# Kernel optimization log

Hardware: AMD Instinct MI355X
Metric: run time of the kernel (lower is better)

The kernel has to match this reference:

```python
import jax, jax.numpy as jnp
import numpy as np

B, W, F, H = 2048, 64, 128, 128


def setup_inputs() -> dict:
    key = jax.random.key(0)
    ks = jax.random.split(key, 23)
    n = lambda k, shape: jax.random.normal(k, shape, dtype=jnp.float32) * 0.05
    return dict(
        X=jax.random.normal(ks[0], (B, W, F), dtype=jnp.float32),
        # InputAttention: linear1 (W+2H -> W), linear2 (W -> 1)
        ia_W1=n(ks[1], (W, W + 2 * H)), ia_b1=n(ks[2], (W,)),
        ia_W2=n(ks[3], (1, W)), ia_b2=n(ks[4], (1,)),
        # encoder LSTMCell(F, H)
        enc_Wih=n(ks[5], (4 * H, F)), enc_Whh=n(ks[6], (4 * H, H)),
        enc_bih=n(ks[7], (4 * H,)), enc_bhh=n(ks[8], (4 * H,)),
        # TemporalAttention: linear1 (3H -> H), linear2 (H -> 1)
        ta_W1=n(ks[9], (H, 3 * H)), ta_b1=n(ks[10], (H,)),
        ta_W2=n(ks[11], (1, H)), ta_b2=n(ks[12], (1,)),
        # decoder LSTMCell(1, H)
        dec_Wih=n(ks[13], (4 * H, 1)), dec_Whh=n(ks[14], (4 * H, H)),
        dec_bih=n(ks[15], (4 * H,)), dec_bhh=n(ks[16], (4 * H,)),
        # output heads
        l1_W=n(ks[17], (1, 1 + H)), l1_b=n(ks[18], (1,)),
        l2_W=n(ks[19], (H, 2 * H)), l2_b=n(ks[20], (H,)),
        l3_W=n(ks[21], (1, H)), l3_b=n(ks[22], (1,)),
    )


def _lstm_cell(x, h, c, Wih, Whh, bih, bhh):
    g = x @ Wih.T + bih + h @ Whh.T + bhh
    i, f, gg, o = jnp.split(g, 4, axis=-1)
    c_new = jax.nn.sigmoid(f) * c + jax.nn.sigmoid(i) * jnp.tanh(gg)
    h_new = jax.nn.sigmoid(o) * jnp.tanh(c_new)
    return h_new, c_new


def reference(X, ia_W1, ia_b1, ia_W2, ia_b2,
              enc_Wih, enc_Whh, enc_bih, enc_bhh,
              ta_W1, ta_b1, ta_W2, ta_b2,
              dec_Wih, dec_Whh, dec_bih, dec_bhh,
              l1_W, l1_b, l2_W, l2_b, l3_W, l3_b):
    Bsz, Wlen, Fdim = X.shape
    Hdim = enc_Whh.shape[1]
    Xf = jnp.transpose(X, (2, 0, 1))  # [F, B, W] (feature-major view for input attention)

    # ---- encoder with input attention ----
    def enc_step(carry, xt):  # xt: [B, F]
        h, c = carry
        hr = jnp.broadcast_to(h[None], (Fdim, Bsz, Hdim))
        cr = jnp.broadcast_to(c[None], (Fdim, Bsz, Hdim))
        u = jnp.tanh(jnp.concatenate([Xf, hr, cr], axis=-1) @ ia_W1.T + ia_b1)  # [F,B,W]
        e = u @ ia_W2.T + ia_b2                                                  # [F,B,1]
        alpha = jax.nn.softmax(e, axis=0)[..., 0].T                              # [B,F]
        h_new, c_new = _lstm_cell(alpha * xt, h, c, enc_Wih, enc_Whh, enc_bih, enc_bhh)
        return (h_new, c_new), h_new

    z = jnp.zeros((Bsz, Hdim), dtype=X.dtype)
    (_, _), Hs = jax.lax.scan(enc_step, (z, z), jnp.transpose(X, (1, 0, 2)))  # Hs: [W,B,H]
    # dropout: eval mode (identity)

    # ---- decoder with temporal attention ----
    def dec_step(carry, _):
        d, ds, out = carry
        dr = jnp.broadcast_to(d[None], Hs.shape)
        dsr = jnp.broadcast_to(ds[None], Hs.shape)
        v = jnp.tanh(jnp.concatenate([Hs, dr, dsr], axis=-1) @ ta_W1.T + ta_b1)  # [W,B,H]
        l = v @ ta_W2.T + ta_b2                                                   # [W,B,1]
        beta = jax.nn.softmax(l, axis=0)
        ct = jnp.sum(beta * Hs, axis=0)                                           # [B,H]
        yt = jnp.concatenate([out, ct], axis=-1) @ l1_W.T + l1_b                  # [B,1]
        d_new, ds_new = _lstm_cell(yt, d, ds, dec_Wih, dec_Whh, dec_bih, dec_bhh)
        o = jnp.concatenate([ct, d_new], axis=-1) @ l2_W.T + l2_b
        out_new = jax.nn.sigmoid(o @ l3_W.T + l3_b)                               # [B,1]
        return (d_new, ds_new, out_new), None

    out0 = jnp.zeros((Bsz, 1), dtype=X.dtype)
    (_, _, output), _ = jax.lax.scan(dec_step, (z, z, out0), None, length=Wlen)
    return output
```

## Files before the change

### kernel.cpp

```cpp
#include <hip/hip_runtime.h>
#include <hip/hip_fp16.h>
#include <stdint.h>

typedef unsigned int uint;
typedef unsigned short ushort;

#define NB 2048
#define NW 64
#define NF 128
#define NH 128

typedef __attribute__((ext_vector_type(8))) short s8v;
typedef __attribute__((ext_vector_type(8))) _Float16 h8v;
typedef __attribute__((ext_vector_type(4))) float f4v;

#define MFMA16(a, b, c) __builtin_amdgcn_mfma_f32_16x16x32_bf16((a), (b), (c), 0, 0, 0)
#define MFMAH(a, b, c)  __builtin_amdgcn_mfma_f32_16x16x32_f16((a), (b), (c), 0, 0, 0)

union H8 { h8v v; __half2 h2[4]; uint4 u4; ushort us[8]; };

__device__ __forceinline__ float bfl(uint u){ return __uint_as_float(u << 16); }
__device__ __forceinline__ float bfh(uint u){ return __uint_as_float(u & 0xffff0000u); }
__device__ __forceinline__ ushort f2bf(float f){
  uint u = __float_as_uint(f);
  u += 0x7fffu + ((u >> 16) & 1u);
  return (ushort)(u >> 16);
}
__device__ __forceinline__ float bf2f(ushort s){ return __uint_as_float(((uint)s) << 16); }

__device__ __forceinline__ float fast_tanh(float x){
  float e = __expf(x + x);
  return 1.f - 2.f * __builtin_amdgcn_rcpf(e + 1.f);
}
__device__ __forceinline__ float fast_sig(float x){
  return __builtin_amdgcn_rcpf(1.f + __expf(-x));
}
__device__ __forceinline__ ushort expo_h(float x){
  return __half_as_ushort(__float2half(__expf(x + x)));
}

__device__ __forceinline__ s8v packW(const float* p){
  s8v r;
  #pragma unroll
  for (int i = 0; i < 8; ++i) r[i] = (short)f2bf(p[i]);
  return r;
}

__global__ __launch_bounds__(256) void k_upre(const float* __restrict__ X,
                                              const float* __restrict__ iaW1,
                                              ushort* __restrict__ Eenc){
  __shared__ __align__(16) float sXT[128*68];
  const int tid = threadIdx.x, lane = tid & 63, wave = tid >> 6, g = lane >> 4;
  int b = blockIdx.x;
  const float* Xb = X + (size_t)b*NW*NF;
  for (int i = tid; i < NW*NF; i += 256){
    int j = i >> 7, f = i & 127;
    sXT[f*68 + j] = Xb[i];
  }
  s8v bw[2];
  {
    int w = wave*16 + (lane & 15);
    #pragma unroll
    for (int kb = 0; kb < 2; ++kb) bw[kb] = packW(iaW1 + w*320 + kb*32 + g*8);
  }
  __syncthreads();
  ushort* outb = Eenc + (size_t)b*NF*NW;
  int w = wave*16 + (lane & 15);
  #pragma unroll
  for (int mt = 0; mt < 8; ++mt){
    int f = mt*16 + (lane & 15);
    f4v acc = {0.f,0.f,0.f,0.f};
    #pragma unroll
    for (int kb = 0; kb < 2; ++kb){
      const float* p = &sXT[f*68 + kb*32 + g*8];
      s8v a;
      #pragma unroll
      for (int i = 0; i < 8; ++i) a[i] = (short)f2bf(p[i]);
      acc = MFMA16(a, bw[kb], acc);
    }
    int fr = mt*16 + g*4;
    #pragma unroll
    for (int j = 0; j < 4; ++j) outb[(fr + j)*64 + w] = expo_h(acc[j]);
  }
}

__global__ __launch_bounds__(256) void k_vpre(const ushort* __restrict__ Hsb,
                                              const float* __restrict__ taW1,
                                              ushort* __restrict__ Edec,
                                              ushort* __restrict__ HsT){
  __shared__ __align__(16) ushort sH[64*136];
  const int tid = threadIdx.x, lane = tid & 63, wave = tid >> 6, g = lane >> 4;
  int b = blockIdx.x;
  const ushort* Hb = Hsb + (size_t)b*NW*NH;
  for (int i = tid; i < 1024; i += 256){
    int w = i >> 4, c = i & 15;
    *(uint4*)&sH[w*136 + c*8] = *(const uint4*)(Hb + i*8);
  }
  s8v bw[2][4];
  #pragma unroll
  for (int nt = 0; nt < 2; ++nt){
    int h = wave*32 + nt*16 + (lane & 15);
    #pragma unroll
    for (int kb = 0; kb < 4; ++kb)
      bw[nt][kb] = packW(taW1 + h*384 + kb*32 + g*8);
  }
  __syncthreads();
  ushort* ho = HsT + (size_t)b*NH*NW;
  for (int k = 0; k < 32; ++k){
    int i2 = tid + 256*k;
    int h = i2 >> 6, w2 = i2 & 63;
    ho[i2] = sH[w2*136 + h];
  }
  ushort* outb = Edec + (size_t)b*NW*NH;
  #pragma unroll
  for (int mt = 0; mt < 4; ++mt){
    s8v af[4];
    #pragma unroll
    for (int kb = 0; kb < 4; ++kb)
      af[kb] = *(const s8v*)&sH[(mt*16 + (lane&15))*136 + kb*32 + g*8];
    #pragma unroll
    for (int nt = 0; nt < 2; ++nt){
      f4v acc = {0.f,0.f,0.f,0.f};
      #pragma unroll
      for (int kb = 0; kb < 4; ++kb) acc = MFMA16(af[kb], bw[nt][kb], acc);
      int h = wave*32 + nt*16 + (lane&15);
      int wr = mt*16 + g*4;
      #pragma unroll
      for (int j = 0; j < 4; ++j) outb[(wr + j)*128 + h] = expo_h(acc[j]);
    }
  }
}

__global__ __launch_bounds__(512, 2) void k_enc(
    const float* __restrict__ X, const float* __restrict__ iaW1,
    const float* __restrict__ iab1, const float* __restrict__ iaW2,
    const float* __restrict__ encWih, const float* __restrict__ encWhh,
    const float* __restrict__ encbih, const float* __restrict__ encbhh,
    const ushort* __restrict__ Eenc, ushort* __restrict__ Hsb){
  __shared__ __align__(16) ushort sUp[65536];
  __shared__ __align__(16) ushort sAB[16*264];
  __shared__ __align__(16) ushort uhc_h[8*64];
  __shared__ __align__(16) float  xrow[8*128];

  const int tid = threadIdx.x, lane = tid & 63, wave = tid >> 6, g = lane >> 4;
  const int bbase = blockIdx.x * 8;
  const int n16 = wave*16 + (lane & 15);

  for (int i = tid; i < 16*264; i += 512) sAB[i] = 0;
  {
    const ushort* up0 = Eenc + (size_t)bbase*NF*NW;
    #pragma unroll
    for (int k = 0; k < 16; ++k){
      int c = tid + k*512;
      int f = (c >> 3) & 127, s = c & 7;
      uint4 v = *(const uint4*)(up0 + (size_t)c*8);
      *(uint4*)((char*)sUp + (c>>3)*128 + ((s ^ (f & 7)) << 4)) = v;
    }
  }
  float bias_r[4];
  #pragma unroll
  for (int gg = 0; gg < 4; ++gg)
    bias_r[gg] = encbih[gg*128 + n16] + encbhh[gg*128 + n16];
  float b1_r = iab1[n16 & 63];
  float c_r[4] = {0.f, 0.f, 0.f, 0.f};
  s8v bwC[4][8];
  #pragma unroll
  for (int gg = 0; gg < 4; ++gg){
    int j = gg*128 + n16;
    #pragma unroll
    for (int kc = 0; kc < 8; ++kc){
      const float* p = (kc < 4) ? (encWih + j*128 + kc*32) : (encWhh + j*128 + (kc-4)*32);
      bwC[gg][kc] = packW(p + g*8);
    }
  }
  s8v bwA[8];
  if (wave < 4){
    #pragma unroll
    for (int kc = 0; kc < 8; ++kc){
      int col = (kc < 4) ? (192 + kc*32) : (64 + (kc-4)*32);
      bwA[kc] = packW(iaW1 + n16*320 + col + g*8);
    }
  }
  H8 w2f[2];
  #pragma unroll
  for (int kb = 0; kb < 2; ++kb)
    #pragma unroll
    for (int i = 0; i < 8; ++i)
      w2f[kb].v[i] = (_Float16)iaW2[kb*32 + g*8 + i];
  __syncthreads();

  for (int t = 0; t < NW; ++t){
    {
      const float* Xr = X + ((size_t)(bbase + wave)*NW + t)*NF;
      xrow[wave*128 + lane] = Xr[lane];
      xrow[wave*128 + 64 + lane] = Xr[64 + lane];
    }
    s8v aT[8];
    #pragma unroll
    for (int kc = 0; kc < 8; ++kc)
      aT[kc] = *(const s8v*)((const char*)sAB + (lane&15)*528 + kc*64 + g*16);
    if (wave < 4){
      f4v acc = {0.f,0.f,0.f,0.f};
      #pragma unroll
      for (int kc = 0; kc < 8; ++kc) acc = MFMA16(aT[kc], bwA[kc], acc);
      if (lane < 32){
        int mb = g*4;
        #pragma unroll
        for (int j = 0; j < 4; ++j) uhc_h[(mb+j)*64 + n16] = expo_h(acc[j] + b1_r);
      }
    }
    __syncthreads();

    {
      int bb = wave;
      const char* Eb = (const char*)sUp + bb*16384;
      H8 sv[2];
      #pragma unroll
      for (int kb = 0; kb < 2; ++kb)
        sv[kb].u4 = *(const uint4*)((const char*)uhc_h + bb*128 + kb*64 + g*16);
      __half2 one2 = __float2half2_rn(1.f);
      f4v Mc[8];
      #pragma unroll
      for (int ft = 0; ft < 8; ++ft){
        int f = ft*16 + (lane & 15);
        const char* rowp = Eb + f*128;
        f4v acc = {0.f,0.f,0.f,0.f};
        #pragma unroll
        for (int kb = 0; kb < 2; ++kb){
          H8 e, a;
          e.v = *(const h8v*)(rowp + (((kb*4 + g) ^ (f & 7)) << 4));
          #pragma unroll
          for (int q = 0; q < 4; ++q) a.h2[q] = h2rcp(__hfma2(e.h2[q], sv[kb].h2[q], one2));
          acc = MFMAH(a.v, w2f[kb].v, acc);
        }
        Mc[ft] = acc;
      }
      float xs[8][4]; float ssum = 0.f;
      #pragma unroll
      for (int ft = 0; ft < 8; ++ft)
        #pragma unroll
        for (int r = 0; r < 4; ++r){ float x = __expf(-2.f*Mc[ft][r]); xs[ft][r] = x; ssum += x; }
      ssum += __shfl_xor(ssum, 16, 64);
      ssum += __shfl_xor(ssum, 32, 64);
      float inv = __builtin_amdgcn_rcpf(ssum);
      if ((lane & 15) == 0){
        #pragma unroll
        for (int ft = 0; ft < 8; ++ft){
          int f0 = ft*16 + g*4;
          float4 Xv = *(const float4*)&xrow[bb*128 + f0];
          uint lo = (uint)f2bf(xs[ft][0]*inv*Xv.x) | ((uint)f2bf(xs[ft][1]*inv*Xv.y) << 16);
          uint hi = (uint)f2bf(xs[ft][2]*inv*Xv.z) | ((uint)f2bf(xs[ft][3]*inv*Xv.w) << 16);
          *(uint2*)((char*)sAB + bb*528 + f0*2) = make_uint2(lo, hi);
        }
      }
    }
    __syncthreads();

    s8v aX[4];
    #pragma unroll
    for (int kc = 0; kc < 4; ++kc)
      aX[kc] = *(const s8v*)((const char*)sAB + (lane&15)*528 + kc*64 + g*16);
    __syncthreads();

    {
      f4v acc[4];
      #pragma unroll
      for (int gg = 0; gg < 4; ++gg) acc[gg] = (f4v){0.f,0.f,0.f,0.f};
      #pragma unroll
      for (int kc = 0; kc < 8; ++kc){
        s8v af = (kc < 4) ? aX[kc] : aT[kc];
        #pragma unroll
        for (int gg = 0; gg < 4; ++gg) acc[gg] = MFMA16(af, bwC[gg][kc], acc[gg]);
      }
      if (lane < 32){
        int mb = g*4;
        #pragma unroll
        for (int j = 0; j < 4; ++j){
          int m = mb + j;
          float gi = acc[0][j] + bias_r[0];
          float gf = acc[1][j] + bias_r[1];
          float gg2 = acc[2][j] + bias_r[2];
          float go = acc[3][j] + bias_r[3];
          float cold = c_r[j];
          float cn = fast_sig(gf)*cold + fast_sig(gi)*fast_tanh(gg2);
          float hn = fast_sig(go)*fast_tanh(cn);
          c_r[j] = cn;
          sAB[m*264 + n16] = f2bf(cn);
          sAB[m*264 + 128 + n16] = f2bf(hn);
          Hsb[((size_t)(bbase + m)*NW + t)*NH + n16] = f2bf(hn);
        }
      }
    }
    __syncthreads();
  }
}

__global__ __launch_bounds__(512, 2) void k_dec(
    const float* __restrict__ taW1, const float* __restrict__ tab1,
    const float* __restrict__ taW2,
    const float* __restrict__ decWih, const float* __restrict__ decWhh,
    const float* __restrict__ decbih, const float* __restrict__ decbhh,
    const float* __restrict__ l1W, const float* __restrict__ l1b,
    const float* __restrict__ l2W, const float* __restrict__ l2b,
    const float* __restrict__ l3W, const float* __restrict__ l3b,
    const ushort* __restrict__ Edec, const ushort* __restrict__ HsT,
    float* __restrict__ out){
  __shared__ __align__(16) ushort sVp[65536];
  __shared__ __align__(16) ushort sAB[16*264];
  __shared__ __align__(16) ushort sCT[16*136];
  __shared__ __align__(16) ushort vd_h[8*128];
  __shared__ __align__(16) ushort lb_bf[8*64];
  __shared__ __align__(16) float  op_s[8][8];
  __shared__ __align__(16) float  yt_s[8];

  const int tid = threadIdx.x, lane = tid & 63, wave = tid >> 6, g = lane >> 4;
  const int bbase = blockIdx.x * 8;
  const int n16 = wave*16 + (lane & 15);

  for (int i = tid; i < 16*264; i += 512) sAB[i] = 0;
  for (int i = tid; i < 16*136; i += 512) sCT[i] = 0;
  {
    const ushort* vp0 = Edec + (size_t)bbase*NW*NH;
    #pragma unroll
    for (int k = 0; k < 16; ++k){
      int c = tid + k*512;
      int w = (c >> 4) & 63, s = c & 15;
      uint4 v = *(const uint4*)(vp0 + (size_t)c*8);
      *(uint4*)((char*)sVp + (c >> 4)*256 + ((s ^ (w & 15)) << 4)) = v;
    }
  }
  float bias_r[4], wih_r[4];
  #pragma unroll
  for (int gg = 0; gg < 4; ++gg){
    bias_r[gg] = decbih[gg*128 + n16] + decbhh[gg*128 + n16];
    wih_r[gg]  = decWih[gg*128 + n16];
  }
  float tab1_r = tab1[n16];
  float l2b_r  = l2b[n16];
  float l3w_r  = l3W[n16];
  float l1w0 = l1W[0], l1b0 = l1b[0], l3b0 = l3b[0];
  float cds_r[4] = {0.f, 0.f, 0.f, 0.f};
  s8v bwA[8];
  #pragma unroll
  for (int kc = 0; kc < 8; ++kc)
    bwA[kc] = packW(taW1 + n16*384 + 128 + kc*32 + g*8);
  s8v bwD[4][4];
  #pragma unroll
  for (int gg = 0; gg < 4; ++gg){
    int j = gg*128 + n16;
    #pragma unroll
    for (int kc = 0; kc < 4; ++kc)
      bwD[gg][kc] = packW(decWhh + j*128 + kc*32 + g*8);
  }
  s8v bwF[8];
  #pragma unroll
  for (int kc = 0; kc < 8; ++kc)
    bwF[kc] = packW(l2W + n16*256 + kc*32 + g*8);
  H8 w2df[4];
  #pragma unroll
  for (int kb = 0; kb < 4; ++kb)
    #pragma unroll
    for (int i = 0; i < 8; ++i)
      w2df[kb].v[i] = (_Float16)taW2[kb*32 + g*8 + i];
  float l1w[8];
  #pragma unroll
  for (int ht = 0; ht < 8; ++ht) l1w[ht] = l1W[1 + ht*16 + (lane & 15)];
  __syncthreads();

  for (int t = 0; t < NW; ++t){
    s8v aT[8];
    #pragma unroll
    for (int kc = 0; kc < 8; ++kc)
      aT[kc] = *(const s8v*)((const char*)sAB + (lane&15)*528 + kc*64 + g*16);
    {
      f4v acc = {0.f,0.f,0.f,0.f};
      #pragma unroll
      for (int kc = 0; kc < 8; ++kc) acc = MFMA16(aT[kc], bwA[kc], acc);
      if (lane < 32){
        int mb = g*4;
        #pragma unroll
        for (int j = 0; j < 4; ++j) vd_h[(mb+j)*128 + n16] = expo_h(acc[j] + tab1_r);
      }
    }
    __syncthreads();

    {
      int bb = wave;
      const ushort* hb = HsT + (size_t)(bbase + bb)*NH*NW;
      s8v hbf[8][2];
      #pragma unroll
      for (int ht = 0; ht < 8; ++ht){
        int h = ht*16 + (lane & 15);
        #pragma unroll
        for (int kb = 0; kb < 2; ++kb)
          hbf[ht][kb] = *(const s8v*)(hb + h*64 + kb*32 + g*8);
      }
      const char* Eb = (const char*)sVp + bb*16384;
      H8 sv[4];
      #pragma unroll
      for (int kb = 0; kb < 4; ++kb)
        sv[kb].u4 = *(const uint4*)((const char*)vd_h + bb*256 + kb*64 + g*16);
      __half2 one2 = __float2half2_rn(1.f);
      f4v Mc[4];
      #pragma unroll
      for (int wt = 0; wt < 4; ++wt){
        int w = wt*16 + (lane & 15);
        const char* rowp = Eb + w*256;
        f4v acc = {0.f,0.f,0.f,0.f};
        #pragma unroll
        for (int kb = 0; kb < 4; ++kb){
          H8 e, a;
          e.v = *(const h8v*)(rowp + (((kb*4 + g) ^ (w & 15)) << 4));
          #pragma unroll
          for (int q = 0; q < 4; ++q) a.h2[q] = h2rcp(__hfma2(e.h2[q], sv[kb].h2[q], one2));
          acc = MFMAH(a.v, w2df[kb].v, acc);
        }
        Mc[wt] = acc;
      }
      float xs[4][4]; float ssum = 0.f;
      #pragma unroll
      for (int wt = 0; wt < 4; ++wt)
        #pragma unroll
        for (int r = 0; r < 4; ++r){ float x = __expf(-2.f*Mc[wt][r]); xs[wt][r] = x; ssum += x; }
      ssum += __shfl_xor(ssum, 16, 64);
      ssum += __shfl_xor(ssum, 32, 64);
      float inv = __builtin_amdgcn_rcpf(ssum);
      if ((lane & 15) == 0){
        #pragma unroll
        for (int wt = 0; wt < 4; ++wt){
          int w0 = wt*16 + g*4;
          uint lo = (uint)f2bf(xs[wt][0]*inv) | ((uint)f2bf(xs[wt][1]*inv) << 16);
          uint hi = (uint)f2bf(xs[wt][2]*inv) | ((uint)f2bf(xs[wt][3]*inv) << 16);
          *(uint2*)((char*)lb_bf + bb*128 + w0*2) = make_uint2(lo, hi);
        }
      }
      s8v ba[2];
      #pragma unroll
      for (int kb = 0; kb < 2; ++kb)
        ba[kb] = *(const s8v*)((const char*)lb_bf + bb*128 + kb*64 + g*16);
      float p = 0.f;
      #pragma unroll
      for (int ht = 0; ht < 8; ++ht){
        f4v acc = {0.f,0.f,0.f,0.f};
        #pragma unroll
        for (int kb = 0; kb < 2; ++kb) acc = MFMA16(ba[kb], hbf[ht][kb], acc);
        float ctv = acc[0];
        if (lane < 16) sCT[bb*136 + ht*16 + (lane&15)] = f2bf(ctv);
        p += l1w[ht] * ctv;
      }
      p += __shfl_xor(p, 1, 64);
      p += __shfl_xor(p, 2, 64);
      p += __shfl_xor(p, 4, 64);
      p += __shfl_xor(p, 8, 64);
      if (lane == 0) yt_s[bb] = p + l1b0;
    }
    __syncthreads();

    {
      f4v g4[4];
      #pragma unroll
      for (int gg = 0; gg < 4; ++gg) g4[gg] = (f4v){0.f,0.f,0.f,0.f};
      #pragma unroll
      for (int kc = 0; kc < 4; ++kc){
        #pragma unroll
        for (int gg = 0; gg < 4; ++gg) g4[gg] = MFMA16(aT[kc], bwD[gg][kc], g4[gg]);
      }
      if (lane < 32){
        int mb = g*4;
        float4 so = make_float4(0.f, 0.f, 0.f, 0.f);
        #pragma unroll
        for (int w = 0; w < 8; ++w){
          float4 v = *(const float4*)((const char*)op_s + w*32 + g*16);
          so.x += v.x; so.y += v.y; so.z += v.z; so.w += v.w;
        }
        float soa[4] = {so.x, so.y, so.z, so.w};
        #pragma unroll
        for (int j = 0; j < 4; ++j){
          int m = mb + j;
          float outp = (t == 0) ? 0.f : fast_sig(soa[j] + l3b0);
          float yt = yt_s[m] + l1w0*outp;
          float gi = g4[0][j] + bias_r[0] + wih_r[0]*yt;
          float gf = g4[1][j] + bias_r[1] + wih_r[1]*yt;
          float gg2 = g4[2][j] + bias_r[2] + wih_r[2]*yt;
          float go = g4[3][j] + bias_r[3] + wih_r[3]*yt;
          float cold = cds_r[j];
          float cn = fast_sig(gf)*cold + fast_sig(gi)*fast_tanh(gg2);
          float hn = fast_sig(go)*fast_tanh(cn);
          cds_r[j] = cn;
          sAB[m*264 + n16] = f2bf(hn);
          sAB[m*264 + 128 + n16] = f2bf(cn);
        }
      }
    }
    __syncthreads();

    {
      f4v of = {0.f,0.f,0.f,0.f};
      #pragma unroll
      for (int kc = 0; kc < 4; ++kc){
        s8v af = *(const s8v*)((const char*)sCT + (lane&15)*272 + kc*64 + g*16);
        of = MFMA16(af, bwF[kc], of);
      }
      #pragma unroll
      for (int kc = 4; kc < 8; ++kc){
        s8v af = *(const s8v*)((const char*)sAB + (lane&15)*528 + (kc-4)*64 + g*16);
        of = MFMA16(af, bwF[kc], of);
      }
      float p0 = l3w_r*(of[0] + l2b_r);
      float p1 = l3w_r*(of[1] + l2b_r);
      float p2 = l3w_r*(of[2] + l2b_r);
      float p3 = l3w_r*(of[3] + l2b_r);
      #pragma unroll
      for (int off = 1; off <= 8; off <<= 1){
        p0 += __shfl_xor(p0, off, 64);
        p1 += __shfl_xor(p1, off, 64);
        p2 += __shfl_xor(p2, off, 64);
        p3 += __shfl_xor(p3, off, 64);
      }
      if ((lane & 15) == 0 && lane < 32){
        *(float4*)((char*)op_s + wave*32 + g*16) = make_float4(p0, p1, p2, p3);
      }
    }
  }
  __syncthreads();
  if (tid < 8){
    float s = 0.f;
    #pragma unroll
    for (int w = 0; w < 8; ++w) s += op_s[w][tid];
    out[bbase + tid] = fast_sig(s + l3b0);
  }
}

extern "C" void kernel_launch(void* const* d_in, const int* in_sizes, int n_in,
                              void* d_out, int out_size, void* d_ws, size_t ws_size,
                              hipStream_t stream){
  const float* X      = (const float*)d_in[0];
  const float* iaW1   = (const float*)d_in[1];
  const float* iab1   = (const float*)d_in[2];
  const float* iaW2   = (const float*)d_in[3];
  const float* encWih = (const float*)d_in[5];
  const float* encWhh = (const float*)d_in[6];
  const float* encbih = (const float*)d_in[7];
  const float* encbhh = (const float*)d_in[8];
  const float* taW1   = (const float*)d_in[9];
  const float* tab1   = (const float*)d_in[10];
  const float* taW2   = (const float*)d_in[11];
  const float* decWih = (const float*)d_in[13];
  const float* decWhh = (const float*)d_in[14];
  const float* decbih = (const float*)d_in[15];
  const float* decbhh = (const float*)d_in[16];
  const float* l1W    = (const float*)d_in[17];
  const float* l1b    = (const float*)d_in[18];
  const float* l2W    = (const float*)d_in[19];
  const float* l2b    = (const float*)d_in[20];
  const float* l3W    = (const float*)d_in[21];
  const float* l3b    = (const float*)d_in[22];

  char* ws = (char*)d_ws;
  ushort* Eenc = (ushort*)(ws);
  ushort* Hsb  = (ushort*)(ws + 33554432);
  ushort* HsT  = (ushort*)(ws + 2*33554432);
  ushort* Edec = Eenc;

  k_upre<<<dim3(2048), dim3(256), 0, stream>>>(X, iaW1, Eenc);
  k_enc<<<dim3(256), dim3(512), 0, stream>>>(X, iaW1, iab1, iaW2,
                                             encWih, encWhh, encbih, encbhh,
                                             Eenc, Hsb);
  k_vpre<<<dim3(2048), dim3(256), 0, stream>>>(Hsb, taW1, Edec, HsT);
  k_dec<<<dim3(256), dim3(512), 0, stream>>>(taW1, tab1, taW2,
                                             decWih, decWhh, decbih, decbhh,
                                             l1W, l1b, l2W, l2b, l3W, l3b,
                                             Edec, HsT, (float*)d_out);
}
```

Before: 1.153 ms.

## Prefetch next X row, drop a barrier, hoist Hs fragments in decoder

```diff
diff --git a/kernel.cpp b/kernel.cpp
--- a/kernel.cpp
+++ b/kernel.cpp
@@ -19,14 +19,11 @@
 
 union H8 { h8v v; __half2 h2[4]; uint4 u4; ushort us[8]; };
 
-__device__ __forceinline__ float bfl(uint u){ return __uint_as_float(u << 16); }
-__device__ __forceinline__ float bfh(uint u){ return __uint_as_float(u & 0xffff0000u); }
 __device__ __forceinline__ ushort f2bf(float f){
   uint u = __float_as_uint(f);
   u += 0x7fffu + ((u >> 16) & 1u);
   return (ushort)(u >> 16);
 }
-__device__ __forceinline__ float bf2f(ushort s){ return __uint_as_float(((uint)s) << 16); }
 
 __device__ __forceinline__ float fast_tanh(float x){
   float e = __expf(x + x);
@@ -139,6 +136,7 @@
     const ushort* __restrict__ Eenc, ushort* __restrict__ Hsb){
   __shared__ __align__(16) ushort sUp[65536];
   __shared__ __align__(16) ushort sAB[16*264];
+  __shared__ __align__(16) ushort sXt[16*264];
   __shared__ __align__(16) ushort uhc_h[8*64];
   __shared__ __align__(16) float  xrow[8*128];
 
@@ -146,7 +144,7 @@
   const int bbase = blockIdx.x * 8;
   const int n16 = wave*16 + (lane & 15);
 
-  for (int i = tid; i < 16*264; i += 512) sAB[i] = 0;
+  for (int i = tid; i < 16*264; i += 512){ sAB[i] = 0; sXt[i] = 0; }
   {
     const ushort* up0 = Eenc + (size_t)bbase*NF*NW;
     #pragma unroll
@@ -187,13 +185,20 @@
     #pragma unroll
     for (int i = 0; i < 8; ++i)
       w2f[kb].v[i] = (_Float16)iaW2[kb*32 + g*8 + i];
+  {
+    const float* Xr = X + ((size_t)(bbase + wave)*NW + 0)*NF;
+    xrow[wave*128 + lane] = Xr[lane];
+    xrow[wave*128 + 64 + lane] = Xr[64 + lane];
+  }
   __syncthreads();
 
   for (int t = 0; t < NW; ++t){
-    {
-      const float* Xr = X + ((size_t)(bbase + wave)*NW + t)*NF;
-      xrow[wave*128 + lane] = Xr[lane];
-      xrow[wave*128 + 64 + lane] = Xr[64 + lane];
+    float xn0, xn1;
+    {
+      int tn = (t + 1) & 63;
+      const float* Xr = X + ((size_t)(bbase + wave)*NW + tn)*NF;
+      xn0 = Xr[lane];
+      xn1 = Xr[64 + lane];
     }
     s8v aT[8];
     #pragma unroll
@@ -250,19 +255,17 @@
           float4 Xv = *(const float4*)&xrow[bb*128 + f0];
           uint lo = (uint)f2bf(xs[ft][0]*inv*Xv.x) | ((uint)f2bf(xs[ft][1]*inv*Xv.y) << 16);
           uint hi = (uint)f2bf(xs[ft][2]*inv*Xv.z) | ((uint)f2bf(xs[ft][3]*inv*Xv.w) << 16);
-          *(uint2*)((char*)sAB + bb*528 + f0*2) = make_uint2(lo, hi);
+          *(uint2*)((char*)sXt + bb*528 + f0*2) = make_uint2(lo, hi);
         }
       }
     }
     __syncthreads();
 
-    s8v aX[4];
-    #pragma unroll
-    for (int kc = 0; kc < 4; ++kc)
-      aX[kc] = *(const s8v*)((const char*)sAB + (lane&15)*528 + kc*64 + g*16);
-    __syncthreads();
-
-    {
+    {
+      s8v aX[4];
+      #pragma unroll
+      for (int kc = 0; kc < 4; ++kc)
+        aX[kc] = *(const s8v*)((const char*)sXt + (lane&15)*528 + kc*64 + g*16);
       f4v acc[4];
       #pragma unroll
       for (int gg = 0; gg < 4; ++gg) acc[gg] = (f4v){0.f,0.f,0.f,0.f};
@@ -290,6 +293,8 @@
           Hsb[((size_t)(bbase + m)*NW + t)*NH + n16] = f2bf(hn);
         }
       }
+      xrow[wave*128 + lane] = xn0;
+      xrow[wave*128 + 64 + lane] = xn1;
     }
     __syncthreads();
   }
@@ -310,6 +315,7 @@
   __shared__ __align__(16) ushort sCT[16*136];
   __shared__ __align__(16) ushort vd_h[8*128];
   __shared__ __align__(16) ushort lb_bf[8*64];
+  __shared__ __align__(16) ushort sW2h[128];
   __shared__ __align__(16) float  op_s[8][8];
   __shared__ __align__(16) float  yt_s[8];
 
@@ -319,6 +325,7 @@
 
   for (int i = tid; i < 16*264; i += 512) sAB[i] = 0;
   for (int i = tid; i < 16*136; i += 512) sCT[i] = 0;
+  if (tid < 128) sW2h[tid] = __half_as_ushort(__float2half(taW2[tid]));
   {
     const ushort* vp0 = Edec + (size_t)bbase*NW*NH;
     #pragma unroll
@@ -356,15 +363,20 @@
   #pragma unroll
   for (int kc = 0; kc < 8; ++kc)
     bwF[kc] = packW(l2W + n16*256 + kc*32 + g*8);
-  H8 w2df[4];
-  #pragma unroll
-  for (int kb = 0; kb < 4; ++kb)
-    #pragma unroll
-    for (int i = 0; i < 8; ++i)
-      w2df[kb].v[i] = (_Float16)taW2[kb*32 + g*8 + i];
   float l1w[8];
   #pragma unroll
   for (int ht = 0; ht < 8; ++ht) l1w[ht] = l1W[1 + ht*16 + (lane & 15)];
+  s8v hbf[8][2];
+  {
+    const ushort* hb = HsT + (size_t)(bbase + wave)*NH*NW;
+    #pragma unroll
+    for (int ht = 0; ht < 8; ++ht){
+      int h = ht*16 + (lane & 15);
+      #pragma unroll
+      for (int kb = 0; kb < 2; ++kb)
+        hbf[ht][kb] = *(const s8v*)(hb + h*64 + kb*32 + g*8);
+    }
+  }
   __syncthreads();
 
   for (int t = 0; t < NW; ++t){
@@ -386,15 +398,6 @@
 
     {
       int bb = wave;
-      const ushort* hb = HsT + (size_t)(bbase + bb)*NH*NW;
-      s8v hbf[8][2];
-      #pragma unroll
-      for (int ht = 0; ht < 8; ++ht){
-        int h = ht*16 + (lane & 15);
-        #pragma unroll
-        for (int kb = 0; kb < 2; ++kb)
-          hbf[ht][kb] = *(const s8v*)(hb + h*64 + kb*32 + g*8);
-      }
       const char* Eb = (const char*)sVp + bb*16384;
       H8 sv[4];
       #pragma unroll
@@ -409,11 +412,12 @@
         f4v acc = {0.f,0.f,0.f,0.f};
         #pragma unroll
         for (int kb = 0; kb < 4; ++kb){
-          H8 e, a;
+          H8 e, a, wv;
+          wv.u4 = *(const uint4*)&sW2h[kb*32 + g*8];
           e.v = *(const h8v*)(rowp + (((kb*4 + g) ^ (w & 15)) << 4));
           #pragma unroll
           for (int q = 0; q < 4; ++q) a.h2[q] = h2rcp(__hfma2(e.h2[q], sv[kb].h2[q], one2));
-          acc = MFMAH(a.v, w2df[kb].v, acc);
+          acc = MFMAH(a.v, wv.v, acc);
         }
         Mc[wt] = acc;
       }
```

After: 1.229 ms. 1.07x slower.

## Store attention exponent tables in FP8 to halve LDS and raise occupancy

Applied to the files above, without the earlier changes.

```diff
diff --git a/kernel.cpp b/kernel.cpp
--- a/kernel.cpp
+++ b/kernel.cpp
@@ -4,6 +4,7 @@
 
 typedef unsigned int uint;
 typedef unsigned short ushort;
+typedef unsigned char uchar;
 
 #define NB 2048
 #define NW 64
@@ -13,11 +14,14 @@
 typedef __attribute__((ext_vector_type(8))) short s8v;
 typedef __attribute__((ext_vector_type(8))) _Float16 h8v;
 typedef __attribute__((ext_vector_type(4))) float f4v;
+typedef __attribute__((ext_vector_type(2))) float f2v;
+typedef __attribute__((ext_vector_type(2))) _Float16 h2v;
+typedef __attribute__((ext_vector_type(2))) __fp16 p2v;
 
 #define MFMA16(a, b, c) __builtin_amdgcn_mfma_f32_16x16x32_bf16((a), (b), (c), 0, 0, 0)
 #define MFMAH(a, b, c)  __builtin_amdgcn_mfma_f32_16x16x32_f16((a), (b), (c), 0, 0, 0)
 
-union H8 { h8v v; __half2 h2[4]; uint4 u4; ushort us[8]; };
+union H8 { h8v v; __half2 h2[4]; h2v hx[4]; p2v px[4]; uint4 u4; ushort us[8]; };
 
 __device__ __forceinline__ float bfl(uint u){ return __uint_as_float(u << 16); }
 __device__ __forceinline__ float bfh(uint u){ return __uint_as_float(u & 0xffff0000u); }
@@ -26,7 +30,6 @@
   u += 0x7fffu + ((u >> 16) & 1u);
   return (ushort)(u >> 16);
 }
-__device__ __forceinline__ float bf2f(ushort s){ return __uint_as_float(((uint)s) << 16); }
 
 __device__ __forceinline__ float fast_tanh(float x){
   float e = __expf(x + x);
@@ -35,8 +38,24 @@
 __device__ __forceinline__ float fast_sig(float x){
   return __builtin_amdgcn_rcpf(1.f + __expf(-x));
 }
-__device__ __forceinline__ ushort expo_h(float x){
-  return __half_as_ushort(__float2half(__expf(x + x)));
+__device__ __forceinline__ ushort expo_hm(float x){
+  return __half_as_ushort(__float2half(__expf(x + x - 1.f)));
+}
+__device__ __forceinline__ uchar expo_fp8(float x){
+  float e = __expf(x + x + 1.f);
+  return (uchar)(__builtin_amdgcn_cvt_pk_fp8_f32(e, e, 0, false) & 0xff);
+}
+__device__ __forceinline__ H8 fp8x8_to_h8(uint2 ev){
+  H8 r;
+  f2v a = __builtin_amdgcn_cvt_pk_f32_fp8((int)ev.x, false);
+  f2v b = __builtin_amdgcn_cvt_pk_f32_fp8((int)ev.x, true);
+  f2v c = __builtin_amdgcn_cvt_pk_f32_fp8((int)ev.y, false);
+  f2v d = __builtin_amdgcn_cvt_pk_f32_fp8((int)ev.y, true);
+  r.px[0] = __builtin_amdgcn_cvt_pkrtz(a.x, a.y);
+  r.px[1] = __builtin_amdgcn_cvt_pkrtz(b.x, b.y);
+  r.px[2] = __builtin_amdgcn_cvt_pkrtz(c.x, c.y);
+  r.px[3] = __builtin_amdgcn_cvt_pkrtz(d.x, d.y);
+  return r;
 }
 
 __device__ __forceinline__ s8v packW(const float* p){
@@ -48,7 +67,7 @@
 
 __global__ __launch_bounds__(256) void k_upre(const float* __restrict__ X,
                                               const float* __restrict__ iaW1,
-                                              ushort* __restrict__ Eenc){
+                                              uchar* __restrict__ Eenc){
   __shared__ __align__(16) float sXT[128*68];
   const int tid = threadIdx.x, lane = tid & 63, wave = tid >> 6, g = lane >> 4;
   int b = blockIdx.x;
@@ -64,7 +83,7 @@
     for (int kb = 0; kb < 2; ++kb) bw[kb] = packW(iaW1 + w*320 + kb*32 + g*8);
   }
   __syncthreads();
-  ushort* outb = Eenc + (size_t)b*NF*NW;
+  uchar* outb = Eenc + (size_t)b*NF*NW;
   int w = wave*16 + (lane & 15);
   #pragma unroll
   for (int mt = 0; mt < 8; ++mt){
@@ -80,13 +99,13 @@
     }
     int fr = mt*16 + g*4;
     #pragma unroll
-    for (int j = 0; j < 4; ++j) outb[(fr + j)*64 + w] = expo_h(acc[j]);
+    for (int j = 0; j < 4; ++j) outb[(fr + j)*64 + w] = expo_fp8(acc[j]);
   }
 }
 
 __global__ __launch_bounds__(256) void k_vpre(const ushort* __restrict__ Hsb,
                                               const float* __restrict__ taW1,
-                                              ushort* __restrict__ Edec,
+                                              uchar* __restrict__ Edec,
                                               ushort* __restrict__ HsT){
   __shared__ __align__(16) ushort sH[64*136];
   const int tid = threadIdx.x, lane = tid & 63, wave = tid >> 6, g = lane >> 4;
@@ -111,7 +130,7 @@
     int h = i2 >> 6, w2 = i2 & 63;
     ho[i2] = sH[w2*136 + h];
   }
-  ushort* outb = Edec + (size_t)b*NW*NH;
+  uchar* outb = Edec + (size_t)b*NW*NH;
   #pragma unroll
   for (int mt = 0; mt < 4; ++mt){
     s8v af[4];
@@ -126,35 +145,35 @@
       int h = wave*32 + nt*16 + (lane&15);
       int wr = mt*16 + g*4;
       #pragma unroll
-      for (int j = 0; j < 4; ++j) outb[(wr + j)*128 + h] = expo_h(acc[j]);
-    }
-  }
-}
-
-__global__ __launch_bounds__(512, 2) void k_enc(
+      for (int j = 0; j < 4; ++j) outb[(wr + j)*128 + h] = expo_fp8(acc[j]);
+    }
+  }
+}
+
+__global__ __launch_bounds__(512, 4) void k_enc(
     const float* __restrict__ X, const float* __restrict__ iaW1,
     const float* __restrict__ iab1, const float* __restrict__ iaW2,
     const float* __restrict__ encWih, const float* __restrict__ encWhh,
     const float* __restrict__ encbih, const float* __restrict__ encbhh,
-    const ushort* __restrict__ Eenc, ushort* __restrict__ Hsb){
-  __shared__ __align__(16) ushort sUp[65536];
-  __shared__ __align__(16) ushort sAB[16*264];
+    const uchar* __restrict__ Eenc, ushort* __restrict__ Hsb){
+  __shared__ __align__(16) uchar  sUp[65536];
+  __shared__ __align__(16) ushort sAB[16*392];
   __shared__ __align__(16) ushort uhc_h[8*64];
-  __shared__ __align__(16) float  xrow[8*128];
+  __shared__ __align__(16) ushort xrowb[8*128];
 
   const int tid = threadIdx.x, lane = tid & 63, wave = tid >> 6, g = lane >> 4;
   const int bbase = blockIdx.x * 8;
   const int n16 = wave*16 + (lane & 15);
 
-  for (int i = tid; i < 16*264; i += 512) sAB[i] = 0;
+  for (int i = tid; i < 16*392; i += 512) sAB[i] = 0;
   {
-    const ushort* up0 = Eenc + (size_t)bbase*NF*NW;
-    #pragma unroll
-    for (int k = 0; k < 16; ++k){
+    const uchar* up0 = Eenc + (size_t)bbase*NF*NW;
+    #pragma unroll
+    for (int k = 0; k < 8; ++k){
       int c = tid + k*512;
-      int f = (c >> 3) & 127, s = c & 7;
-      uint4 v = *(const uint4*)(up0 + (size_t)c*8);
-      *(uint4*)((char*)sUp + (c>>3)*128 + ((s ^ (f & 7)) << 4)) = v;
+      int row = c >> 2, f = row & 127, s = c & 3;
+      uint4 v = *(const uint4*)(up0 + (size_t)c*16);
+      *(uint4*)((char*)sUp + row*64 + ((s ^ (f & 3)) << 4)) = v;
     }
   }
   float bias_r[4];
@@ -187,18 +206,25 @@
     #pragma unroll
     for (int i = 0; i < 8; ++i)
       w2f[kb].v[i] = (_Float16)iaW2[kb*32 + g*8 + i];
+  {
+    const float* Xr = X + ((size_t)(bbase + wave)*NW + 0)*NF;
+    xrowb[wave*128 + lane] = f2bf(Xr[lane]);
+    xrowb[wave*128 + 64 + lane] = f2bf(Xr[64 + lane]);
+  }
   __syncthreads();
 
   for (int t = 0; t < NW; ++t){
+    float xn0, xn1;
     {
-      const float* Xr = X + ((size_t)(bbase + wave)*NW + t)*NF;
-      xrow[wave*128 + lane] = Xr[lane];
-      xrow[wave*128 + 64 + lane] = Xr[64 + lane];
+      int tn = (t + 1) & 63;
+      const float* Xr = X + ((size_t)(bbase + wave)*NW + tn)*NF;
+      xn0 = Xr[lane];
+      xn1 = Xr[64 + lane];
     }
     s8v aT[8];
     #pragma unroll
     for (int kc = 0; kc < 8; ++kc)
-      aT[kc] = *(const s8v*)((const char*)sAB + (lane&15)*528 + kc*64 + g*16);
+      aT[kc] = *(const s8v*)((const char*)sAB + (lane&15)*784 + kc*64 + g*16);
     if (wave < 4){
       f4v acc = {0.f,0.f,0.f,0.f};
       #pragma unroll
@@ -206,14 +232,14 @@
       if (lane < 32){
         int mb = g*4;
         #pragma unroll
-        for (int j = 0; j < 4; ++j) uhc_h[(mb+j)*64 + n16] = expo_h(acc[j] + b1_r);
+        for (int j = 0; j < 4; ++j) uhc_h[(mb+j)*64 + n16] = expo_hm(acc[j] + b1_r);
       }
     }
     __syncthreads();
 
     {
       int bb = wave;
-      const char* Eb = (const char*)sUp + bb*16384;
+      const char* Eb = (const char*)sUp + bb*8192;
       H8 sv[2];
       #pragma unroll
       for (int kb = 0; kb < 2; ++kb)
@@ -223,12 +249,14 @@
       #pragma unroll
       for (int ft = 0; ft < 8; ++ft){
         int f = ft*16 + (lane & 15);
-        const char* rowp = Eb + f*128;
+        const char* rowp = Eb + f*64;
         f4v acc = {0.f,0.f,0.f,0.f};
         #pragma unroll
         for (int kb = 0; kb < 2; ++kb){
-          H8 e, a;
-          e.v = *(const h8v*)(rowp + (((kb*4 + g) ^ (f & 7)) << 4));
+          int gr = kb*4 + g;
+          uint2 ev = *(const uint2*)(rowp + ((((gr >> 1) ^ (f & 3)) << 4) + ((gr & 1) << 3)));
+          H8 e = fp8x8_to_h8(ev);
+          H8 a;
           #pragma unroll
           for (int q = 0; q < 4; ++q) a.h2[q] = h2rcp(__hfma2(e.h2[q], sv[kb].h2[q], one2));
           acc = MFMAH(a.v, w2f[kb].v, acc);
@@ -247,22 +275,20 @@
         #pragma unroll
         for (int ft = 0; ft < 8; ++ft){
           int f0 = ft*16 + g*4;
-          float4 Xv = *(const float4*)&xrow[bb*128 + f0];
-          uint lo = (uint)f2bf(xs[ft][0]*inv*Xv.x) | ((uint)f2bf(xs[ft][1]*inv*Xv.y) << 16);
-          uint hi = (uint)f2bf(xs[ft][2]*inv*Xv.z) | ((uint)f2bf(xs[ft][3]*inv*Xv.w) << 16);
-          *(uint2*)((char*)sAB + bb*528 + f0*2) = make_uint2(lo, hi);
+          uint2 xw = *(const uint2*)&xrowb[bb*128 + f0];
+          uint lo = (uint)f2bf(xs[ft][0]*inv*bfl(xw.x)) | ((uint)f2bf(xs[ft][1]*inv*bfh(xw.x)) << 16);
+          uint hi = (uint)f2bf(xs[ft][2]*inv*bfl(xw.y)) | ((uint)f2bf(xs[ft][3]*inv*bfh(xw.y)) << 16);
+          *(uint2*)((char*)sAB + bb*784 + 512 + f0*2) = make_uint2(lo, hi);
         }
       }
     }
     __syncthreads();
 
-    s8v aX[4];
-    #pragma unroll
-    for (int kc = 0; kc < 4; ++kc)
-      aX[kc] = *(const s8v*)((const char*)sAB + (lane&15)*528 + kc*64 + g*16);
-    __syncthreads();
-
     {
+      s8v aX[4];
+      #pragma unroll
+      for (int kc = 0; kc < 4; ++kc)
+        aX[kc] = *(const s8v*)((const char*)sAB + (lane&15)*784 + 512 + kc*64 + g*16);
       f4v acc[4];
       #pragma unroll
       for (int gg = 0; gg < 4; ++gg) acc[gg] = (f4v){0.f,0.f,0.f,0.f};
@@ -285,17 +311,19 @@
           float cn = fast_sig(gf)*cold + fast_sig(gi)*fast_tanh(gg2);
           float hn = fast_sig(go)*fast_tanh(cn);
           c_r[j] = cn;
-          sAB[m*264 + n16] = f2bf(cn);
-          sAB[m*264 + 128 + n16] = f2bf(hn);
+          sAB[m*392 + n16] = f2bf(cn);
+          sAB[m*392 + 128 + n16] = f2bf(hn);
           Hsb[((size_t)(bbase + m)*NW + t)*NH + n16] = f2bf(hn);
         }
       }
+      xrowb[wave*128 + lane] = f2bf(xn0);
+      xrowb[wave*128 + 64 + lane] = f2bf(xn1);
     }
     __syncthreads();
   }
 }
 
-__global__ __launch_bounds__(512, 2) void k_dec(
+__global__ __launch_bounds__(512, 4) void k_dec(
     const float* __restrict__ taW1, const float* __restrict__ tab1,
     const float* __restrict__ taW2,
     const float* __restrict__ decWih, const float* __restrict__ decWhh,
@@ -303,11 +331,11 @@
     const float* __restrict__ l1W, const float* __restrict__ l1b,
     const float* __restrict__ l2W, const float* __restrict__ l2b,
     const float* __restrict__ l3W, const float* __restrict__ l3b,
-    const ushort* __restrict__ Edec, const ushort* __restrict__ HsT,
+    const uchar* __restrict__ Edec, const ushort* __restrict__ HsT,
     float* __restrict__ out){
-  __shared__ __align__(16) ushort sVp[65536];
+  __shared__ __align__(16) uchar  sVp[65536];
   __shared__ __align__(16) ushort sAB[16*264];
-  __shared__ __align__(16) ushort sCT[16*136];
+  __shared__ __align__(16) ushort sCT[8*136];
   __shared__ __align__(16) ushort vd_h[8*128];
   __shared__ __align__(16) ushort lb_bf[8*64];
   __shared__ __align__(16) float  op_s[8][8];
@@ -318,15 +346,14 @@
   const int n16 = wave*16 + (lane & 15);
 
   for (int i = tid; i < 16*264; i += 512) sAB[i] = 0;
-  for (int i = tid; i < 16*136; i += 512) sCT[i] = 0;
   {
-    const ushort* vp0 = Edec + (size_t)bbase*NW*NH;
-    #pragma unroll
-    for (int k = 0; k < 16; ++k){
+    const uchar* vp0 = Edec + (size_t)bbase*NW*NH;
+    #pragma unroll
+    for (int k = 0; k < 8; ++k){
       int c = tid + k*512;
-      int w = (c >> 4) & 63, s = c & 15;
-      uint4 v = *(const uint4*)(vp0 + (size_t)c*8);
-      *(uint4*)((char*)sVp + (c >> 4)*256 + ((s ^ (w & 15)) << 4)) = v;
+      int row = c >> 3, w = row & 63, s = c & 7;
+      uint4 v = *(const uint4*)(vp0 + (size_t)c*16);
+      *(uint4*)((char*)sVp + row*128 + ((s ^ (w & 7)) << 4)) = v;
     }
   }
   float bias_r[4], wih_r[4];
@@ -379,7 +406,7 @@
       if (lane < 32){
         int mb = g*4;
         #pragma unroll
-        for (int j = 0; j < 4; ++j) vd_h[(mb+j)*128 + n16] = expo_h(acc[j] + tab1_r);
+        for (int j = 0; j < 4; ++j) vd_h[(mb+j)*128 + n16] = expo_hm(acc[j] + tab1_r);
       }
     }
     __syncthreads();
@@ -395,7 +422,7 @@
         for (int kb = 0; kb < 2; ++kb)
           hbf[ht][kb] = *(const s8v*)(hb + h*64 + kb*32 + g*8);
       }
-      const char* Eb = (const char*)sVp + bb*16384;
+      const char* Eb = (const char*)sVp + bb*8192;
       H8 sv[4];
       #pragma unroll
       for (int kb = 0; kb < 4; ++kb)
@@ -405,12 +432,14 @@
       #pragma unroll
       for (int wt = 0; wt < 4; ++wt){
         int w = wt*16 + (lane & 15);
-        const char* rowp = Eb + w*256;
+        const char* rowp = Eb + w*128;
         f4v acc = {0.f,0.f,0.f,0.f};
         #pragma unroll
         for (int kb = 0; kb < 4; ++kb){
-          H8 e, a;
-          e.v = *(const h8v*)(rowp + (((kb*4 + g) ^ (w & 15)) << 4));
+          int gr = kb*4 + g;
+          uint2 ev = *(const uint2*)(rowp + ((((gr >> 1) ^ (w & 7)) << 4) + ((gr & 1) << 3)));
+          H8 e = fp8x8_to_h8(ev);
+          H8 a;
           #pragma unroll
           for (int q = 0; q < 4; ++q) a.h2[q] = h2rcp(__hfma2(e.h2[q], sv[kb].h2[q], one2));
           acc = MFMAH(a.v, w2df[kb].v, acc);
@@ -557,10 +586,10 @@
   const float* l3b    = (const float*)d_in[22];
 
   char* ws = (char*)d_ws;
-  ushort* Eenc = (ushort*)(ws);
+  uchar*  Eenc = (uchar*)(ws);
   ushort* Hsb  = (ushort*)(ws + 33554432);
   ushort* HsT  = (ushort*)(ws + 2*33554432);
-  ushort* Edec = Eenc;
+  uchar*  Edec = Eenc;
 
   k_upre<<<dim3(2048), dim3(256), 0, stream>>>(X, iaW1, Eenc);
   k_enc<<<dim3(256), dim3(512), 0, stream>>>(X, iaW1, iab1, iaW2,
```

Measured after the change: 2.802 ms. 143% more time.
